# Kernel tuning notes

Measured on AMD Instinct MI355X. Metric: run time of the kernel, lower is better.

## Reference

```python
import jax, jax.numpy as jnp
import numpy as np

NUM_ITERATIONS = 3


def squash(s, eps=1e-9):
    # s: [..., dim]; squash along last axis
    n2 = jnp.sum(s * s, axis=-1, keepdims=True)
    scale = n2 / (1.0 + n2) / jnp.sqrt(n2 + eps)
    return scale * s


def setup_inputs() -> dict:
    key = jax.random.key(0)
    k1, k2 = jax.random.split(key)
    B, T, R, C, D_OUT, D_IN = 16, 64, 256, 16, 16, 16
    ui = jax.random.normal(k1, (B, T, D_IN), dtype=jnp.float32)
    W = jax.random.normal(k2, (1, R, C, D_OUT, D_IN), dtype=jnp.float32)
    return {"ui": ui, "W": W}


def reference(ui, W):
    # Faithful to torch.einsum('brcdo,btrci->btrco', W, ui_expanded):
    # sums over d (out_dim) AND i (in_dim); output last axis is W's last axis (in_dim).
    # The expand() calls are pure broadcasts, so we contract the unexpanded tensors.
    u_hat = jnp.einsum('rcdo,bti->btrco', W[0], ui)  # [B,T,R,C,in_dim]
    B, R, C = u_hat.shape[0], u_hat.shape[2], u_hat.shape[3]
    b_ij = jnp.zeros((B, R, C), dtype=u_hat.dtype)
    v_j = None
    for r in range(NUM_ITERATIONS):
        c_ij = jax.nn.softmax(b_ij, axis=2)                      # [B,R,C]
        s_j = jnp.einsum('brc,btrco->btco', c_ij, u_hat)         # sum over routes
        v_j = squash(s_j)                                        # [B,T,C,in_dim]
        if r < NUM_ITERATIONS - 1:
            # agreement: sum over last dim then over time (dim=1)
            b_ij = b_ij + jnp.einsum('btrco,btco->brc', u_hat, v_j)
    return v_j  # matches torch v_j.squeeze(2): [B,T,C,in_dim]
```

## Files before the change

kernel.cpp:

```cpp
#include <hip/hip_runtime.h>
#include <math.h>


#define OFF_WT 0

__device__ __forceinline__ float squash_scale(float n2) {
    return n2 / (1.0f + n2) * rsqrtf(n2 + 1e-9f);
}

__global__ void __launch_bounds__(256) k1_prep(const float* __restrict__ W,
                                               float* __restrict__ ws) {
    __shared__ float sh[4 * 256];
    const int tid = threadIdx.x, bid = blockIdx.x;
    const int rr = tid >> 6;
    const int l = tid & 63;
    const int c = l >> 2, o4 = l & 3;
    const int r = bid * 4 + rr;
    const float* bp = W + r * 4096 + c * 256 + o4 * 4;
    float4 a = make_float4(0.f, 0.f, 0.f, 0.f);
#pragma unroll
    for (int d = 0; d < 16; ++d) {
        const float4 w = *(const float4*)(bp + d * 16);
        a.x += w.x; a.y += w.y; a.z += w.z; a.w += w.w;
    }
    const int co = c * 16 + o4 * 4;
    sh[rr * 256 + co + 0] = a.x;
    sh[rr * 256 + co + 1] = a.y;
    sh[rr * 256 + co + 2] = a.z;
    sh[rr * 256 + co + 3] = a.w;
    __syncthreads();
    {
        const int co2 = tid;
        float4 t;
        t.x = sh[0 * 256 + co2];
        t.y = sh[1 * 256 + co2];
        t.z = sh[2 * 256 + co2];
        t.w = sh[3 * 256 + co2];
        *(float4*)(ws + OFF_WT + co2 * 256 + bid * 4) = t;
    }
}

__global__ void __launch_bounds__(1024, 4) k2_route(
    const float* __restrict__ ui, const float* __restrict__ ws,
    float* __restrict__ out)
{
    __shared__ __align__(16) float bijL[16][260];
    __shared__ __align__(16) float cijL[16][260];
    const int b = blockIdx.x, tid = threadIdx.x;
    const int w = tid >> 6, l = tid & 63;

    float4 wreg[16];
#pragma unroll
    for (int o = 0; o < 16; ++o)
        wreg[o] = *(const float4*)(ws + OFF_WT + (w * 16 + o) * 256 + 4 * l);

    float us;
    {
        const float4* u4 = (const float4*)(ui + b * 1024 + l * 16);
        const float4 a = u4[0], e = u4[1], f = u4[2], g = u4[3];
        us = ((a.x + a.y) + (a.z + a.w)) + ((e.x + e.y) + (e.z + e.w))
           + ((f.x + f.y) + (f.z + f.w)) + ((g.x + g.y) + (g.z + g.w));
    }

    float S[16];
    float4 bijv = make_float4(0.f, 0.f, 0.f, 0.f);

#pragma unroll
    for (int it = 0; it < 3; ++it) {
        if (it == 0) {
#pragma unroll
            for (int o = 0; o < 16; ++o)
                S[o] = (wreg[o].x + wreg[o].y) + (wreg[o].z + wreg[o].w);
        } else {
            const float4 c4 = *(const float4*)(&cijL[w][4 * l]);
#pragma unroll
            for (int o = 0; o < 16; ++o)
                S[o] = c4.x * wreg[o].x + c4.y * wreg[o].y
                     + c4.z * wreg[o].z + c4.w * wreg[o].w;
        }
#pragma unroll
        for (int off = 1; off < 64; off <<= 1)
#pragma unroll
            for (int o = 0; o < 16; ++o) S[o] += __shfl_xor(S[o], off, 64);
        if (it == 0)
#pragma unroll
            for (int o = 0; o < 16; ++o) S[o] *= (1.0f / 16.0f);

        if (it < 2) {
            float ns = 0.f;
#pragma unroll
            for (int o = 0; o < 16; ++o) ns += S[o] * S[o];
            const float us2 = us * us;
            float ts = us2 * squash_scale(us2 * ns);
#pragma unroll
            for (int off = 1; off < 64; off <<= 1) ts += __shfl_xor(ts, off, 64);

            float4 g4 = make_float4(0.f, 0.f, 0.f, 0.f);
#pragma unroll
            for (int o = 0; o < 16; ++o) {
                g4.x += wreg[o].x * S[o]; g4.y += wreg[o].y * S[o];
                g4.z += wreg[o].z * S[o]; g4.w += wreg[o].w * S[o];
            }
            bijv.x += g4.x * ts; bijv.y += g4.y * ts;
            bijv.z += g4.z * ts; bijv.w += g4.w * ts;
            *(float4*)(&bijL[w][4 * l]) = bijv;
            __syncthreads();

            {
                const int r = tid >> 2, j = tid & 3;
                float v0 = bijL[4 * j + 0][r], v1 = bijL[4 * j + 1][r];
                float v2 = bijL[4 * j + 2][r], v3 = bijL[4 * j + 3][r];
                float m = fmaxf(fmaxf(v0, v1), fmaxf(v2, v3));
                m = fmaxf(m, __shfl_xor(m, 1, 4));
                m = fmaxf(m, __shfl_xor(m, 2, 4));
                const float e0 = __expf(v0 - m), e1 = __expf(v1 - m);
                const float e2 = __expf(v2 - m), e3 = __expf(v3 - m);
                float z = (e0 + e1) + (e2 + e3);
                z += __shfl_xor(z, 1, 4);
                z += __shfl_xor(z, 2, 4);
                const float inv = 1.0f / z;
                cijL[4 * j + 0][r] = e0 * inv;
                cijL[4 * j + 1][r] = e1 * inv;
                cijL[4 * j + 2][r] = e2 * inv;
                cijL[4 * j + 3][r] = e3 * inv;
            }
            __syncthreads();
        }
    }

    {
        float ns = 0.f;
#pragma unroll
        for (int o = 0; o < 16; ++o) ns += S[o] * S[o];
        const float n2 = us * us * ns;
        const float f = squash_scale(n2) * us;
        float4* o4 = (float4*)(out + (((b * 64 + l) * 16 + w) << 4));
#pragma unroll
        for (int q = 0; q < 4; ++q) {
            float4 ov;
            ov.x = f * S[q * 4 + 0];
            ov.y = f * S[q * 4 + 1];
            ov.z = f * S[q * 4 + 2];
            ov.w = f * S[q * 4 + 3];
            o4[q] = ov;
        }
    }
}

extern "C" void kernel_launch(void* const* d_in, const int* in_sizes, int n_in,
                              void* d_out, int out_size, void* d_ws, size_t ws_size,
                              hipStream_t stream) {
    const float* ui = (const float*)d_in[0];
    const float* W  = (const float*)d_in[1];
    float* out = (float*)d_out;
    float* ws  = (float*)d_ws;

    k1_prep<<<64, 256, 0, stream>>>(W, ws);
    k2_route<<<16, 1024, 0, stream>>>(ui, ws, out);
}
```

Before: 29.48 us.

## Fuse prep and routing kernels with flag-based inter-block sync and per-thread softmax

Merges the W-reduction prep kernel and the routing kernel into one launch. Sixteen producer blocks write the reduced weights and publish a release-ordered flag; sixteen consumer blocks spin on those flags before loading the weights. The routing softmax is also restructured: each thread computes max and sum over the 16 capsules itself from a double-buffered shared array, which removes the transpose-style softmax pass and one barrier per iteration. The aim is to remove a kernel launch and a barrier per iteration. In exchange it relies on co-residency of all blocks, spin-waits, and never resets the flags, so later calls may read the workspace while it is being rewritten.

```diff
diff --git a/kernel.cpp b/kernel.cpp
--- a/kernel.cpp
+++ b/kernel.cpp
@@ -2,57 +2,60 @@
 #include <math.h>
 
 
-#define OFF_WT 0
+#define OFF_WT   0
+#define OFF_FLAG 65536
+#define MAGIC    0x5AC3F00Du
 
 __device__ __forceinline__ float squash_scale(float n2) {
     return n2 / (1.0f + n2) * rsqrtf(n2 + 1e-9f);
 }
 
-__global__ void __launch_bounds__(256) k1_prep(const float* __restrict__ W,
-                                               float* __restrict__ ws) {
-    __shared__ float sh[4 * 256];
-    const int tid = threadIdx.x, bid = blockIdx.x;
-    const int rr = tid >> 6;
-    const int l = tid & 63;
-    const int c = l >> 2, o4 = l & 3;
-    const int r = bid * 4 + rr;
-    const float* bp = W + r * 4096 + c * 256 + o4 * 4;
-    float4 a = make_float4(0.f, 0.f, 0.f, 0.f);
+__global__ void __launch_bounds__(1024) caps_fused(
+    const float* __restrict__ ui, const float* __restrict__ W,
+    float* __restrict__ out, float* __restrict__ ws)
+{
+    const int bid = blockIdx.x, tid = threadIdx.x;
+    unsigned* flg = (unsigned*)(ws + OFF_FLAG);
+
+    if (bid < 16) {
+        __shared__ float sh[16 * 256];
+        const int rr = tid >> 6;
+        const int l = tid & 63;
+        const int c = l >> 2, o4 = l & 3;
+        const int r = bid * 16 + rr;
+        const float* bp = W + r * 4096 + c * 256 + o4 * 4;
+        float4 a = make_float4(0.f, 0.f, 0.f, 0.f);
 #pragma unroll
-    for (int d = 0; d < 16; ++d) {
-        const float4 w = *(const float4*)(bp + d * 16);
-        a.x += w.x; a.y += w.y; a.z += w.z; a.w += w.w;
+        for (int d = 0; d < 16; ++d) {
+            const float4 w = *(const float4*)(bp + d * 16);
+            a.x += w.x; a.y += w.y; a.z += w.z; a.w += w.w;
+        }
+        const int co = c * 16 + o4 * 4;
+        sh[rr * 256 + co + 0] = a.x;
+        sh[rr * 256 + co + 1] = a.y;
+        sh[rr * 256 + co + 2] = a.z;
+        sh[rr * 256 + co + 3] = a.w;
+        __syncthreads();
+        {
+            const int co2 = tid >> 2, q = tid & 3;
+            float4 t;
+            t.x = sh[(q * 4 + 0) * 256 + co2];
+            t.y = sh[(q * 4 + 1) * 256 + co2];
+            t.z = sh[(q * 4 + 2) * 256 + co2];
+            t.w = sh[(q * 4 + 3) * 256 + co2];
+            *(float4*)(ws + OFF_WT + co2 * 256 + bid * 16 + q * 4) = t;
+        }
+        __threadfence();
+        __syncthreads();
+        if (tid == 0)
+            __hip_atomic_store(&flg[bid], MAGIC, __ATOMIC_RELEASE,
+                               __HIP_MEMORY_SCOPE_AGENT);
+        return;
     }
-    const int co = c * 16 + o4 * 4;
-    sh[rr * 256 + co + 0] = a.x;
-    sh[rr * 256 + co + 1] = a.y;
-    sh[rr * 256 + co + 2] = a.z;
-    sh[rr * 256 + co + 3] = a.w;
-    __syncthreads();
-    {
-        const int co2 = tid;
-        float4 t;
-        t.x = sh[0 * 256 + co2];
-        t.y = sh[1 * 256 + co2];
-        t.z = sh[2 * 256 + co2];
-        t.w = sh[3 * 256 + co2];
-        *(float4*)(ws + OFF_WT + co2 * 256 + bid * 4) = t;
-    }
-}
 
-__global__ void __launch_bounds__(1024, 4) k2_route(
-    const float* __restrict__ ui, const float* __restrict__ ws,
-    float* __restrict__ out)
-{
-    __shared__ __align__(16) float bijL[16][260];
-    __shared__ __align__(16) float cijL[16][260];
-    const int b = blockIdx.x, tid = threadIdx.x;
+    __shared__ __align__(16) float bijL[2][16][260];
+    const int b = bid - 16;
     const int w = tid >> 6, l = tid & 63;
-
-    float4 wreg[16];
-#pragma unroll
-    for (int o = 0; o < 16; ++o)
-        wreg[o] = *(const float4*)(ws + OFF_WT + (w * 16 + o) * 256 + 4 * l);
 
     float us;
     {
@@ -61,9 +64,19 @@
         us = ((a.x + a.y) + (a.z + a.w)) + ((e.x + e.y) + (e.z + e.w))
            + ((f.x + f.y) + (f.z + f.w)) + ((g.x + g.y) + (g.z + g.w));
     }
+    while (__hip_atomic_load(&flg[l & 15], __ATOMIC_ACQUIRE,
+                             __HIP_MEMORY_SCOPE_AGENT) != MAGIC) {
+        __builtin_amdgcn_s_sleep(1);
+    }
+
+    float4 wreg[16];
+#pragma unroll
+    for (int o = 0; o < 16; ++o)
+        wreg[o] = *(const float4*)(ws + OFF_WT + (w * 16 + o) * 256 + 4 * l);
 
     float S[16];
     float4 bijv = make_float4(0.f, 0.f, 0.f, 0.f);
+    float4 cij  = make_float4(0.f, 0.f, 0.f, 0.f);
 
 #pragma unroll
     for (int it = 0; it < 3; ++it) {
@@ -72,11 +85,10 @@
             for (int o = 0; o < 16; ++o)
                 S[o] = (wreg[o].x + wreg[o].y) + (wreg[o].z + wreg[o].w);
         } else {
-            const float4 c4 = *(const float4*)(&cijL[w][4 * l]);
 #pragma unroll
             for (int o = 0; o < 16; ++o)
-                S[o] = c4.x * wreg[o].x + c4.y * wreg[o].y
-                     + c4.z * wreg[o].z + c4.w * wreg[o].w;
+                S[o] = cij.x * wreg[o].x + cij.y * wreg[o].y
+                     + cij.z * wreg[o].z + cij.w * wreg[o].w;
         }
 #pragma unroll
         for (int off = 1; off < 64; off <<= 1)
@@ -103,28 +115,27 @@
             }
             bijv.x += g4.x * ts; bijv.y += g4.y * ts;
             bijv.z += g4.z * ts; bijv.w += g4.w * ts;
-            *(float4*)(&bijL[w][4 * l]) = bijv;
+            *(float4*)(&bijL[it][w][4 * l]) = bijv;
             __syncthreads();
 
-            {
-                const int r = tid >> 2, j = tid & 3;
-                float v0 = bijL[4 * j + 0][r], v1 = bijL[4 * j + 1][r];
-                float v2 = bijL[4 * j + 2][r], v3 = bijL[4 * j + 3][r];
-                float m = fmaxf(fmaxf(v0, v1), fmaxf(v2, v3));
-                m = fmaxf(m, __shfl_xor(m, 1, 4));
-                m = fmaxf(m, __shfl_xor(m, 2, 4));
-                const float e0 = __expf(v0 - m), e1 = __expf(v1 - m);
-                const float e2 = __expf(v2 - m), e3 = __expf(v3 - m);
-                float z = (e0 + e1) + (e2 + e3);
-                z += __shfl_xor(z, 1, 4);
-                z += __shfl_xor(z, 2, 4);
-                const float inv = 1.0f / z;
-                cijL[4 * j + 0][r] = e0 * inv;
-                cijL[4 * j + 1][r] = e1 * inv;
-                cijL[4 * j + 2][r] = e2 * inv;
-                cijL[4 * j + 3][r] = e3 * inv;
+            float4 mm = *(const float4*)(&bijL[it][0][4 * l]);
+#pragma unroll
+            for (int cc = 1; cc < 16; ++cc) {
+                const float4 v = *(const float4*)(&bijL[it][cc][4 * l]);
+                mm.x = fmaxf(mm.x, v.x); mm.y = fmaxf(mm.y, v.y);
+                mm.z = fmaxf(mm.z, v.z); mm.w = fmaxf(mm.w, v.w);
             }
-            __syncthreads();
+            float4 z = make_float4(0.f, 0.f, 0.f, 0.f);
+#pragma unroll
+            for (int cc = 0; cc < 16; ++cc) {
+                const float4 v = *(const float4*)(&bijL[it][cc][4 * l]);
+                z.x += __expf(v.x - mm.x); z.y += __expf(v.y - mm.y);
+                z.z += __expf(v.z - mm.z); z.w += __expf(v.w - mm.w);
+            }
+            cij.x = __expf(bijv.x - mm.x) / z.x;
+            cij.y = __expf(bijv.y - mm.y) / z.y;
+            cij.z = __expf(bijv.z - mm.z) / z.z;
+            cij.w = __expf(bijv.w - mm.w) / z.w;
         }
     }
 
@@ -155,6 +166,5 @@
     float* out = (float*)d_out;
     float* ws  = (float*)d_ws;
 
-    k1_prep<<<64, 256, 0, stream>>>(W, ws);
-    k2_route<<<16, 1024, 0, stream>>>(ui, ws, out);
+    caps_fused<<<32, 1024, 0, stream>>>(ui, W, out, ws);
 }
```

After: 38.52 us. +30.7%, slower.
